# Performance work log

Measured on AMD Instinct MI355X. Metric: run time of the kernel, lower is better.

## Reference

```python
import jax, jax.numpy as jnp
import numpy as np

WIDTH = 64
N_LAYERS = 4
K_MAX = 16
DT = 0.05
EPS = 1e-5


def _gelu(x):
    return jax.nn.gelu(x, approximate=False)  # torch nn.GELU default = exact erf


def _pconv(x, w, b):
    # 1x1 conv: x (B,Cin,H,W), w (Cout,Cin), b (Cout,)
    return jnp.einsum('oc,bchw->bohw', w, x) + b[None, :, None, None]


def _spectral_conv(x, wr, wi):
    # Faithful to the original buggy einsum: x_ft is summed over ky before the weight multiply.
    B, C, H, W = x.shape
    x_ft = jnp.fft.rfft2(x, norm='ortho')              # (B,C,H,W//2+1) complex
    k = min(K_MAX, H, W // 2 + 1)
    weights = (wr + 1j * wi)[:, :, :k, :k]             # (Cin,Cout,k,k)
    S = jnp.sum(x_ft[:, :, :k, :k], axis=2)           # (B,Cin,k): sum over ky rows (broadcasted label j)
    blk = jnp.einsum('bik,ijkm->bjkm', S, weights.astype(x_ft.dtype))  # (B,Cout,k,k)
    out_ft = jnp.zeros((B, wr.shape[1], H, W // 2 + 1), dtype=x_ft.dtype)
    out_ft = out_ft.at[:, :, :k, :k].set(blk)
    return jnp.fft.irfft2(out_ft, s=(H, W), norm='ortho')


def _instance_norm(x):
    # InstanceNorm2d(affine=False): per (b,c) normalization over H,W, biased var
    mu = jnp.mean(x, axis=(2, 3), keepdims=True)
    var = jnp.var(x, axis=(2, 3), keepdims=True)
    return (x - mu) * jax.lax.rsqrt(var + EPS)


def _spectral_divergence(J):
    B, _, H, W = J.shape
    Jx_ft = jnp.fft.rfft2(J[:, 0:1], norm='ortho')
    Jy_ft = jnp.fft.rfft2(J[:, 1:2], norm='ortho')
    kx = jnp.fft.fftfreq(W, d=1.0 / W)[: W // 2 + 1]   # integer freqs, cols
    ky = jnp.fft.fftfreq(H, d=1.0 / H)[:H]             # integer freqs, rows
    # torch: kxx,kyy = meshgrid(ky,kx,'ij'); div_ft = 1j*kxx*Jx_ft + 1j*kyy*Jy_ft
    div_ft = 1j * ky[None, None, :, None] * Jx_ft + 1j * kx[None, None, None, :] * Jy_ft
    return jnp.fft.irfft2(div_ft, s=(H, W), norm='ortho')


def setup_inputs() -> dict:
    key = jax.random.key(0)
    ks = jax.random.split(key, 16)
    B, H, W = 8, 256, 256
    scale = 1.0 / (WIDTH * WIDTH)
    return {
        'state': jax.random.normal(ks[0], (B, 3, H, W), jnp.float32),
        'lift_w': 0.1 * jax.random.normal(ks[1], (WIDTH, 3), jnp.float32),
        'lift_b': jnp.zeros((WIDTH,), jnp.float32),
        'sw_real': scale * jax.random.normal(ks[2], (N_LAYERS, WIDTH, WIDTH, K_MAX, K_MAX), jnp.float32),
        'sw_imag': scale * jax.random.normal(ks[3], (N_LAYERS, WIDTH, WIDTH, K_MAX, K_MAX), jnp.float32),
        'pw_w': 0.05 * jax.random.normal(ks[4], (N_LAYERS, WIDTH, WIDTH), jnp.float32),
        'pw_b': jnp.zeros((N_LAYERS, WIDTH), jnp.float32),
        'flux_w1': 0.05 * jax.random.normal(ks[5], (WIDTH, WIDTH), jnp.float32),
        'flux_b1': jnp.zeros((WIDTH,), jnp.float32),
        'flux_w2': 0.05 * jax.random.normal(ks[6], (2, WIDTH), jnp.float32),
        'flux_b2': jnp.zeros((2,), jnp.float32),
        'pol_w1': 0.05 * jax.random.normal(ks[7], (WIDTH, WIDTH), jnp.float32),
        'pol_b1': jnp.zeros((WIDTH,), jnp.float32),
        'pol_w2': 0.05 * jax.random.normal(ks[8], (2, WIDTH), jnp.float32),
        'pol_b2': jnp.zeros((2,), jnp.float32),
    }


def reference(state, lift_w, lift_b, sw_real, sw_imag, pw_w, pw_b,
              flux_w1, flux_b1, flux_w2, flux_b2,
              pol_w1, pol_b1, pol_w2, pol_b2):
    x = _gelu(_pconv(state, lift_w, lift_b))
    for l in range(N_LAYERS):
        res = x
        x = _spectral_conv(x, sw_real[l], sw_imag[l])
        x = _pconv(x, pw_w[l], pw_b[l])
        x = _instance_norm(x)
        x = _gelu(x)
        x = x + res
    J = _pconv(_gelu(_pconv(x, flux_w1, flux_b1)), flux_w2, flux_b2)      # (B,2,H,W)
    dt_rho = -_spectral_divergence(J)                                     # (B,1,H,W)
    dt_P = _pconv(_gelu(_pconv(x, pol_w1, pol_b1)), pol_w2, pol_b2)       # (B,2,H,W)
    dt_state = jnp.concatenate([dt_rho, dt_P], axis=1)
    rho_new = state[:, 0:1] + DT * dt_rho
    P_new = state[:, 1:] + DT * dt_P
    rho_new = jnp.logaddexp(0.0, 10.0 * rho_new) / 10.0  # softplus(beta=10)
    state_pred = jnp.concatenate([rho_new, P_new], axis=1)
    return state_pred, dt_state
```

## Files before the change

### kernel.cpp

```cpp
#include <hip/hip_runtime.h>
#include <math.h>

#define HW 65536
#define TH_ 0.024543692606170259f

typedef __attribute__((ext_vector_type(8))) short bf16x8;
typedef __attribute__((ext_vector_type(4))) float f32x4;

__device__ __forceinline__ float gelu_f(float v){
    float u = fabsf(v)*0.7071067811865476f;
    float t = __builtin_amdgcn_rcpf(fmaf(0.3275911f, u, 1.0f));
    float p = t*fmaf(t, fmaf(t, fmaf(t, fmaf(t, 1.061405429f, -1.453152027f),
                     1.421413741f), -0.284496736f), 0.254829592f);
    float e = __expf(-u*u);
    float erfu = fmaf(-p, e, 1.0f);
    float er = copysignf(erfu, v);
    return 0.5f*v*(1.0f+er);
}

__device__ __forceinline__ short f2bf(float f){
    union { float f; unsigned u; } v; v.f = f;
    unsigned r = (v.u + 0x7FFF + ((v.u >> 16) & 1)) >> 16;
    return (short)r;
}
__device__ __forceinline__ float bf2f(short s){
    union { float f; unsigned u; } v; v.u = ((unsigned)(unsigned short)s) << 16;
    return v.f;
}

__device__ __forceinline__ unsigned cvt_pk_bf16(float lo, float hi){
    unsigned r;
    asm("v_cvt_pk_bf16_f32 %0, %1, %2" : "=v"(r) : "v"(lo), "v"(hi));
    return r;
}

union U8 { bf16x8 v; unsigned u[4]; };

__device__ __forceinline__ void split8(const float* f, bf16x8& H, bf16x8& L){
    U8 h, l;
    #pragma unroll
    for (int p=0;p<4;++p){
        float a = f[2*p], b = f[2*p+1];
        unsigned hp = cvt_pk_bf16(a, b);
        union { unsigned u; float fl; } ua, ub;
        ua.u = hp << 16; ub.u = hp & 0xffff0000u;
        h.u[p] = hp;
        l.u[p] = cvt_pk_bf16(a - ua.fl, b - ub.fl);
    }
    H = h.v; L = l.v;
}

__device__ __forceinline__ void s_partial_atomic(float TrT, float TiT, int w, int lane,
                                                 float* __restrict__ Sdst){
    float c1, s1; sincosf((float)w * TH_, &s1, &c1);
    float Sr[16], Si[16];
    float ck = 1.f, sk = 0.f;
    #pragma unroll
    for (int k=0;k<16;++k){
        Sr[k] = (TrT*ck + TiT*sk) * (1.0f/256.0f);
        Si[k] = (TiT*ck - TrT*sk) * (1.0f/256.0f);
        float nc = ck*c1 - sk*s1;
        sk = ck*s1 + sk*c1;
        ck = nc;
    }
    #pragma unroll
    for (int k=0;k<16;++k){
        #pragma unroll
        for (int off=32; off; off>>=1){
            Sr[k] += __shfl_xor(Sr[k], off, 64);
            Si[k] += __shfl_xor(Si[k], off, 64);
        }
    }
    if (lane < 32){
        float val = (lane & 1) ? Si[lane>>1] : Sr[lane>>1];
        atomicAdd(Sdst + lane, val);
    }
}

__global__ __launch_bounds__(256) void k_init(const float* __restrict__ fw1, const float* __restrict__ qw1,
                                              float* __restrict__ Wf, float* __restrict__ GH,
                                              float* __restrict__ KQ){
    if (blockIdx.x == 4){
        int h = threadIdx.x;
        double gr = 0.0, gi = 0.0;
        for (int ky=0; ky<16; ++ky){
            double a = -2.0*3.14159265358979323846*(double)(ky*h)/256.0;
            gr += cos(a); gi += sin(a);
        }
        GH[2*h] = (float)gr; GH[2*h+1] = (float)gi;
        double kk = 0.0, qq = 0.0;
        for (int k=1; k<128; ++k){
            double s = sin(2.0*3.14159265358979323846*(double)(k*h)/256.0);
            kk += (double)k * s;
            qq += s;
        }
        KQ[h]     = (float)(-kk/128.0);
        KQ[256+h] = (float)( qq/128.0);
        return;
    }
    int t = blockIdx.x*256 + threadIdx.x;
    int lane = t & 63, ks = (t>>6)&1, n = (t>>7)&3, ph = (t>>9)&1;
    int l15 = lane & 15, lg = lane >> 4;
    const float* w1p = ph ? qw1 : fw1;
    int oc = n*16 + l15;
    U8 h, l;
    #pragma unroll
    for (int p=0;p<4;++p){
        float a = w1p[oc*64 + ks*32 + lg*8 + 2*p];
        float b = w1p[oc*64 + ks*32 + lg*8 + 2*p+1];
        short ha = f2bf(a), hb = f2bf(b);
        h.u[p] = ((unsigned)(unsigned short)ha) | (((unsigned)(unsigned short)hb)<<16);
        short la = f2bf(a - bf2f(ha)), lb = f2bf(b - bf2f(hb));
        l.u[p] = ((unsigned)(unsigned short)la) | (((unsigned)(unsigned short)lb)<<16);
    }
    int idx = ((ph*4+n)*2+ks)*64 + lane;
    ((bf16x8*)Wf)[idx] = h.v;
    ((bf16x8*)Wf)[1024 + idx] = l.v;
}

__global__ __launch_bounds__(1024) void k_lift2(const float* __restrict__ st, const float* __restrict__ lw,
                                                const float* __restrict__ lb, const float* __restrict__ GH,
                                                float* __restrict__ x, float* __restrict__ Sout){
    int b = blockIdx.x >> 6, c = blockIdx.x & 63;
    int t = threadIdx.x;
    int w = t & 255, hq = t >> 8;
    __shared__ float sGH[512];
    __shared__ float2 tp[4][256];
    if (t < 512) sGH[t] = GH[t];
    __syncthreads();
    float l0 = lw[c*3], l1 = lw[c*3+1], l2 = lw[c*3+2], lbc = lb[c];
    const float* s0p = st + (size_t)(b*3)*HW;
    float* xp = x + (size_t)blockIdx.x*HW;
    float Tr = 0.f, Ti = 0.f;
    #pragma unroll 4
    for (int i=0; i<64; ++i){
        int h = hq*64 + i;
        int idx = h*256 + w;
        float v = fmaf(l0, s0p[idx], fmaf(l1, s0p[HW+idx], fmaf(l2, s0p[2*HW+idx], lbc)));
        v = gelu_f(v);
        xp[idx] = v;
        Tr = fmaf(sGH[2*h],   v, Tr);
        Ti = fmaf(sGH[2*h+1], v, Ti);
    }
    tp[hq][w] = make_float2(Tr, Ti);
    __syncthreads();
    if (hq == 0){
        float2 a = tp[0][w], b2 = tp[1][w], cc = tp[2][w], d = tp[3][w];
        float TrT = a.x+b2.x+cc.x+d.x, TiT = a.y+b2.y+cc.y+d.y;
        s_partial_atomic(TrT, TiT, w, t & 63, Sout + blockIdx.x*32);
    }
}

__global__ __launch_bounds__(256) void k_mixA(const float* __restrict__ S, const float* __restrict__ wr,
                                              const float* __restrict__ wi, float* __restrict__ A){
    int j = blockIdx.x >> 3, b = blockIdx.x & 7;
    __shared__ float sS[2048];
    for (int t=threadIdx.x; t<2048; t+=256) sS[t] = S[b*2048 + t];
    __syncthreads();
    int km = threadIdx.x, k = km >> 4;
    float ar = 0.f, ai = 0.f;
    const float* wrp = wr + j*256 + km;
    const float* wip = wi + j*256 + km;
    #pragma unroll 4
    for (int i=0;i<64;++i){
        float wrv = wrp[i*16384];
        float wiv = wip[i*16384];
        float2 sv = ((const float2*)sS)[i*16 + k];
        ar += sv.x*wrv - sv.y*wiv;
        ai += sv.x*wiv + sv.y*wrv;
    }
    ((float2*)A)[(b*64 + j)*256 + km] = make_float2(ar, ai);
}

__global__ __launch_bounds__(256) void k_mixB(const float* __restrict__ A, const float* __restrict__ pw,
                                              float* __restrict__ CS){
    int b = blockIdx.x >> 6, o = blockIdx.x & 63;
    int km = threadIdx.x, m = km & 15;
    const float2* Ap = (const float2*)A + b*64*256 + km;
    const float* pwp = pw + o*64;
    float cr=0.f, ci=0.f;
    #pragma unroll 4
    for (int j=0;j<64;++j){
        float p = pwp[j];
        float2 a = Ap[j*256];
        cr = fmaf(p, a.x, cr);
        ci = fmaf(p, a.y, ci);
    }
    float aw = (m==0)? 1.f : 4.f;
    float s = (km==0)? 0.f : aw*(cr*cr + ci*ci);
    #pragma unroll
    for (int off=32; off; off>>=1) s += __shfl_xor(s, off, 64);
    __shared__ float rsum[4];
    __shared__ float sinv;
    if ((threadIdx.x & 63) == 0) rsum[threadIdx.x>>6] = s;
    __syncthreads();
    if (threadIdx.x == 0){
        float var = (rsum[0]+rsum[1]+rsum[2]+rsum[3]) * (1.0f/131072.0f);
        sinv = rsqrtf(var + 1e-5f);
    }
    __syncthreads();
    float alpha = (m==0)? 1.f : 2.f;
    float sc = sinv * alpha * (1.0f/256.0f);
    if (km == 0) cr = 0.f;
    ((float2*)CS)[blockIdx.x*256 + km] = make_float2(cr*sc, ci*sc);
}

template<bool EMIT_S>
__global__ __launch_bounds__(256) void k_synth(const float* __restrict__ CS, float* __restrict__ x,
                                               const float* __restrict__ GH, float* __restrict__ Sout){
    int bo = blockIdx.x >> 2, wt = blockIdx.x & 3;
    int lane = threadIdx.x & 63, wv = threadIdx.x >> 6;
    int w = wt*64 + lane;
    __shared__ float sGH[512];
    __shared__ float2 sV[16][64];
    if (EMIT_S){
        sGH[threadIdx.x] = GH[threadIdx.x];
        sGH[256+threadIdx.x] = GH[256+threadIdx.x];
    }
    const float2* cs = (const float2*)CS + bo*256;
    {
        float Vr[4] = {0.f,0.f,0.f,0.f}, Vi[4] = {0.f,0.f,0.f,0.f};
        float stepc, steps; sincosf((float)w*TH_, &steps, &stepc);
        float pc = 1.f, ps = 0.f;
        for (int m=0;m<16;++m){
            #pragma unroll
            for (int kk=0;kk<4;++kk){
                float2 a = cs[(wv*4+kk)*16 + m];
                Vr[kk] += a.x*pc - a.y*ps;
                Vi[kk] += a.x*ps + a.y*pc;
            }
            float nc = pc*stepc - ps*steps;
            ps = pc*steps + ps*stepc;
            pc = nc;
        }
        #pragma unroll
        for (int kk=0;kk<4;++kk) sV[wv*4+kk][lane] = make_float2(Vr[kk], Vi[kk]);
    }
    __syncthreads();
    int h0 = wv*16;
    float rc[16], rs[16], qr[16], qi[16];
    #pragma unroll
    for (int k=0;k<16;++k){
        float2 v = sV[k][lane];
        sincosf((float)k*TH_, &rs[k], &rc[k]);
        float c0, s0; sincosf((float)(k*h0)*TH_, &s0, &c0);
        qr[k] = v.x*c0 - v.y*s0;
        qi[k] = v.x*s0 + v.y*c0;
    }
    float* xp = x + ((size_t)bo << 16);
    float Tr = 0.f, Ti = 0.f;
    for (int i=0;i<16;++i){
        float y0=0.f,y1=0.f,y2=0.f,y3=0.f;
        #pragma unroll
        for (int k=0;k<16;++k){
            float re = qr[k], im = qi[k];
            y0 += re;
            if ((k&3)==0)      { y1 += re; y2 += re; y3 += re; }
            else if ((k&3)==1) { y1 -= im; y2 -= re; y3 += im; }
            else if ((k&3)==2) { y1 -= re; y2 += re; y3 -= re; }
            else               { y1 += im; y2 -= re; y3 -= im; }
        }
        #pragma unroll
        for (int k=1;k<16;++k){
            float nr = qr[k]*rc[k] - qi[k]*rs[k];
            qi[k]    = qr[k]*rs[k] + qi[k]*rc[k];
            qr[k] = nr;
        }
        int p0 = (h0+i)*256 + w;
        float x0 = xp[p0], x1 = xp[p0+16384], x2 = xp[p0+32768], x3 = xp[p0+49152];
        float n0 = gelu_f(y0) + x0;
        float n1 = gelu_f(y1) + x1;
        float n2 = gelu_f(y2) + x2;
        float n3 = gelu_f(y3) + x3;
        xp[p0]       = n0;
        xp[p0+16384] = n1;
        xp[p0+32768] = n2;
        xp[p0+49152] = n3;
        if (EMIT_S){
            int h = h0+i;
            Tr = fmaf(sGH[2*h],     n0, Tr);  Ti = fmaf(sGH[2*h+1],     n0, Ti);
            Tr = fmaf(sGH[2*h+128], n1, Tr);  Ti = fmaf(sGH[2*h+129],   n1, Ti);
            Tr = fmaf(sGH[2*h+256], n2, Tr);  Ti = fmaf(sGH[2*h+257],   n2, Ti);
            Tr = fmaf(sGH[2*h+384], n3, Tr);  Ti = fmaf(sGH[2*h+385],   n3, Ti);
        }
    }
    if (EMIT_S){
        __shared__ float2 tpart[4][64];
        tpart[wv][lane] = make_float2(Tr, Ti);
        __syncthreads();
        if (wv == 0){
            float2 a = tpart[0][lane], b2 = tpart[1][lane];
            float2 c = tpart[2][lane], d = tpart[3][lane];
            float TrT = a.x+b2.x+c.x+d.x, TiT = a.y+b2.y+c.y+d.y;
            s_partial_atomic(TrT, TiT, w, lane, Sout + bo*32);
        }
    }
}

__global__ __launch_bounds__(256) void k_heads(const float* __restrict__ x,
        const float* __restrict__ Wf, const float* __restrict__ st,
        const float* __restrict__ fb1, const float* __restrict__ fw2, const float* __restrict__ fb2,
        const float* __restrict__ qb1, const float* __restrict__ qw2, const float* __restrict__ qb2,
        float* __restrict__ J, float* __restrict__ outp){
    __shared__ bf16x8 sWf[2048];
    for (int t = threadIdx.x; t < 2048; t += 256)
        sWf[t] = ((const bf16x8*)Wf)[t];
    __syncthreads();

    int wv = threadIdx.x >> 6, lane = threadIdx.x & 63;
    int l15 = lane & 15, lg = lane >> 4;
    int px0 = blockIdx.x*128 + wv*32;
    int b = px0 >> 16;
    int hwbase = px0 & (HW-1);
    const float* xb = x + (size_t)b*64*HW;

    bf16x8 Ahi[2][2], Alo[2][2];
    #pragma unroll
    for (int mt=0; mt<2; ++mt){
        int px = hwbase + mt*16 + l15;
        #pragma unroll
        for (int ks=0; ks<2; ++ks){
            float f[8];
            #pragma unroll
            for (int j=0; j<8; ++j)
                f[j] = xb[(size_t)((ks*32 + lg*8 + j))*HW + px];
            split8(f, Ahi[mt][ks], Alo[mt][ks]);
        }
    }

    #pragma unroll
    for (int ph=0; ph<2; ++ph){
        const float* b1p = ph ? qb1 : fb1;
        const float* w2p = ph ? qw2 : fw2;
        const float* b2p = ph ? qb2 : fb2;

        float p0[8], p1[8];
        #pragma unroll
        for (int t=0;t<8;++t){ p0[t]=0.f; p1[t]=0.f; }

        for (int n=0; n<4; ++n){
            int oc = n*16 + l15;
            float bias = b1p[oc];
            float w2a = w2p[oc], w2b = w2p[64+oc];
            int base = ((ph*4+n)*2)*64 + lane;
            bf16x8 Bhi0 = sWf[base];
            bf16x8 Bhi1 = sWf[base + 64];
            bf16x8 Blo0 = sWf[1024 + base];
            bf16x8 Blo1 = sWf[1024 + base + 64];
            #pragma unroll
            for (int mt=0; mt<2; ++mt){
                f32x4 d = {0.f,0.f,0.f,0.f};
                d = __builtin_amdgcn_mfma_f32_16x16x32_bf16(Ahi[mt][0], Bhi0, d, 0,0,0);
                d = __builtin_amdgcn_mfma_f32_16x16x32_bf16(Ahi[mt][0], Blo0, d, 0,0,0);
                d = __builtin_amdgcn_mfma_f32_16x16x32_bf16(Alo[mt][0], Bhi0, d, 0,0,0);
                d = __builtin_amdgcn_mfma_f32_16x16x32_bf16(Ahi[mt][1], Bhi1, d, 0,0,0);
                d = __builtin_amdgcn_mfma_f32_16x16x32_bf16(Ahi[mt][1], Blo1, d, 0,0,0);
                d = __builtin_amdgcn_mfma_f32_16x16x32_bf16(Alo[mt][1], Bhi1, d, 0,0,0);
                #pragma unroll
                for (int r=0;r<4;++r){
                    float g = gelu_f(d[r] + bias);
                    p0[mt*4+r] = fmaf(w2a, g, p0[mt*4+r]);
                    p1[mt*4+r] = fmaf(w2b, g, p1[mt*4+r]);
                }
            }
        }
        #pragma unroll
        for (int t=0;t<8;++t){
            #pragma unroll
            for (int off=1; off<16; off<<=1){
                p0[t] += __shfl_xor(p0[t], off, 64);
                p1[t] += __shfl_xor(p1[t], off, 64);
            }
        }
        float bo0 = b2p[0], bo1 = b2p[1];
        if (ph == 0){
            if (l15 == 0){
                float* plane = J + ((size_t)(b*2 + 0))*HW;
                #pragma unroll
                for (int mt=0; mt<2; ++mt){
                    int px = hwbase + mt*16 + lg*4;
                    float4 v; v.x=p0[mt*4+0]+bo0; v.y=p0[mt*4+1]+bo0; v.z=p0[mt*4+2]+bo0; v.w=p0[mt*4+3]+bo0;
                    *(float4*)(plane + px) = v;
                }
            } else if (l15 == 1){
                float* plane = J + ((size_t)(b*2 + 1))*HW;
                #pragma unroll
                for (int mt=0; mt<2; ++mt){
                    int px = hwbase + mt*16 + lg*4;
                    float4 v; v.x=p1[mt*4+0]+bo1; v.y=p1[mt*4+1]+bo1; v.z=p1[mt*4+2]+bo1; v.w=p1[mt*4+3]+bo1;
                    *(float4*)(plane + px) = v;
                }
            }
        } else {
            if (l15 < 2){
                const float* pv = (l15==0)? p0 : p1;
                float bN = (l15==0)? bo0 : bo1;
                const float* plane_st  = st   + ((size_t)(b*3+1+l15))*HW;
                float* plane_pred      = outp + ((size_t)(b*3+1+l15))*HW;
                float* plane_dt        = outp + 1572864 + ((size_t)(b*3+1+l15))*HW;
                #pragma unroll
                for (int mt=0; mt<2; ++mt){
                    int px = hwbase + mt*16 + lg*4;
                    float4 sv = *(const float4*)(plane_st + px);
                    float4 dt, pd;
                    dt.x = pv[mt*4+0]+bN; dt.y = pv[mt*4+1]+bN;
                    dt.z = pv[mt*4+2]+bN; dt.w = pv[mt*4+3]+bN;
                    pd.x = fmaf(0.05f, dt.x, sv.x); pd.y = fmaf(0.05f, dt.y, sv.y);
                    pd.z = fmaf(0.05f, dt.z, sv.z); pd.w = fmaf(0.05f, dt.w, sv.w);
                    *(float4*)(plane_pred + px) = pd;
                    *(float4*)(plane_dt + px)   = dt;
                }
            }
        }
    }
}

__global__ __launch_bounds__(256) void k_convH(const float* __restrict__ J, const float* __restrict__ KQ,
                                               float* __restrict__ Dx, float* __restrict__ r){
    int b = blockIdx.x >> 5, wt = blockIdx.x & 31;
    int w0 = wt*8;
    __shared__ float tile[256][12];
    __shared__ float sK[256];
    int t = threadIdx.x;
    sK[t] = KQ[t];
    {
        const float* rp = J + (size_t)(b*2)*HW + t*256 + w0;
        float4 a = *(const float4*)rp;
        float4 bb = *(const float4*)(rp+4);
        tile[t][0]=a.x;  tile[t][1]=a.y;  tile[t][2]=a.z;  tile[t][3]=a.w;
        tile[t][4]=bb.x; tile[t][5]=bb.y; tile[t][6]=bb.z; tile[t][7]=bb.w;
    }
    __syncthreads();
    if (t < 8){
        float acc = 0.f;
        for (int h=0; h<256; ++h) acc += (h & 1)? -tile[h][t] : tile[h][t];
        r[b*256 + w0 + t] = acc;
    }
    float o[8] = {0.f,0.f,0.f,0.f,0.f,0.f,0.f,0.f};
    for (int hp=0; hp<256; ++hp){
        float k = sK[(t - hp) & 255];
        float4 ra = *(const float4*)&tile[hp][0];
        float4 rb = *(const float4*)&tile[hp][4];
        o[0]=fmaf(k, ra.x, o[0]); o[1]=fmaf(k, ra.y, o[1]);
        o[2]=fmaf(k, ra.z, o[2]); o[3]=fmaf(k, ra.w, o[3]);
        o[4]=fmaf(k, rb.x, o[4]); o[5]=fmaf(k, rb.y, o[5]);
        o[6]=fmaf(k, rb.z, o[6]); o[7]=fmaf(k, rb.w, o[7]);
    }
    float* dp = Dx + (size_t)b*HW + t*256 + w0;
    float4 v0; v0.x=o[0]; v0.y=o[1]; v0.z=o[2]; v0.w=o[3];
    float4 v1; v1.x=o[4]; v1.y=o[5]; v1.z=o[6]; v1.w=o[7];
    *(float4*)dp = v0;
    *(float4*)(dp+4) = v1;
}

__global__ __launch_bounds__(256) void k_convW(const float* __restrict__ J, const float* __restrict__ KQ,
                                               const float* __restrict__ Dx, const float* __restrict__ r,
                                               const float* __restrict__ st, float* __restrict__ outp){
    int b = blockIdx.x >> 5, ht = blockIdx.x & 31;
    int h0 = ht*8;
    __shared__ float rows[8][256];
    __shared__ float sr[256], sK[256], sQ[256];
    int t = threadIdx.x;
    sK[t] = KQ[t];
    sQ[t] = KQ[256+t];
    sr[t] = r[b*256 + t];
    const float* jy = J + (size_t)(b*2+1)*HW;
    #pragma unroll
    for (int i=0;i<8;++i) rows[i][t] = jy[(h0+i)*256 + t];
    __syncthreads();
    float P = 0.f;
    float cv[8] = {0.f,0.f,0.f,0.f,0.f,0.f,0.f,0.f};
    for (int wp=0; wp<256; ++wp){
        int d = (t - wp) & 255;
        float kk = sK[d];
        P = fmaf(sQ[d], sr[wp], P);
        #pragma unroll
        for (int i=0;i<8;++i) cv[i] = fmaf(kk, rows[i][wp], cv[i]);
    }
    const float* s0p = st + (size_t)(b*3)*HW;
    const float* dxp = Dx + (size_t)b*HW;
    float* o_rho = outp + (size_t)(b*3)*HW;
    float* o_dt  = outp + 1572864 + (size_t)(b*3)*HW;
    #pragma unroll
    for (int i=0;i<8;++i){
        int h = h0 + i;
        int idx = h*256 + t;
        float corr = ((h & 1)? -0.5f : 0.5f) * P;
        float rho = -(dxp[idx] + cv[i] + corr);
        float tt = 10.f*fmaf(0.05f, rho, s0p[idx]);
        float sp = fmaxf(tt, 0.f) + log1pf(expf(-fabsf(tt)));
        o_rho[idx] = 0.1f*sp;
        o_dt[idx]  = rho;
    }
}

extern "C" void kernel_launch(void* const* d_in, const int* in_sizes, int n_in,
                              void* d_out, int out_size, void* d_ws, size_t ws_size,
                              hipStream_t stream){
    const float* state = (const float*)d_in[0];
    const float* lw  = (const float*)d_in[1];
    const float* lb  = (const float*)d_in[2];
    const float* swr = (const float*)d_in[3];
    const float* swi = (const float*)d_in[4];
    const float* pww = (const float*)d_in[5];
    const float* fw1 = (const float*)d_in[7];
    const float* fb1 = (const float*)d_in[8];
    const float* fw2 = (const float*)d_in[9];
    const float* fb2 = (const float*)d_in[10];
    const float* qw1 = (const float*)d_in[11];
    const float* qb1 = (const float*)d_in[12];
    const float* qw2 = (const float*)d_in[13];
    const float* qb2 = (const float*)d_in[14];
    float* outp = (float*)d_out;
    float* ws = (float*)d_ws;

    float* x   = ws;
    float* S   = x   + 33554432;
    float* A   = S   + 65536;
    float* CS  = A   + 262144;
    float* J   = CS  + 262144;
    float* Dx  = J   + 1048576;
    float* rr  = Dx  + 524288;
    float* GH  = rr  + 2048;
    float* KQ  = GH  + 512;
    float* Wf  = KQ  + 512;

    hipLaunchKernelGGL(k_init,  dim3(5), dim3(256), 0, stream, fw1, qw1, Wf, GH, KQ);
    hipMemsetAsync(S, 0, 65536*sizeof(float), stream);
    hipLaunchKernelGGL(k_lift2, dim3(512), dim3(1024), 0, stream, state, lw, lb, GH, x, S);
    for (int l=0; l<4; ++l){
        float* Sl = S + l*16384;
        hipLaunchKernelGGL(k_mixA, dim3(512), dim3(256), 0, stream, Sl,
                           swr + (size_t)l*1048576, swi + (size_t)l*1048576, A);
        hipLaunchKernelGGL(k_mixB, dim3(512), dim3(256), 0, stream, A, pww + l*4096, CS);
        if (l < 3)
            hipLaunchKernelGGL((k_synth<true>),  dim3(2048), dim3(256), 0, stream, CS, x, GH, S + (l+1)*16384);
        else
            hipLaunchKernelGGL((k_synth<false>), dim3(2048), dim3(256), 0, stream, CS, x, GH, S);
    }
    hipLaunchKernelGGL(k_heads, dim3(4096), dim3(256), 0, stream, x,
                       Wf, state, fb1, fw2, fb2, qb1, qw2, qb2, J, outp);
    hipLaunchKernelGGL(k_convH, dim3(256), dim3(256), 0, stream, J, KQ, Dx, rr);
    hipLaunchKernelGGL(k_convW, dim3(256), dim3(256), 0, stream, J, KQ, Dx, rr, state, outp);
}
```

Baseline: 479.8 us.

## Compute inverse row DFT in synth kernel with split-bf16 MFMA against precomputed twiddles

The per-thread rotating-phasor recurrence over 16 modes for the inverse H-direction transform in k_synth is replaced by 16x16x32 bf16 MFMAs. A precomputed cos/sin twiddle table, split into hi/lo bf16 parts, is multiplied against the mode coefficients using three MFMAs per tile to keep near-fp32 accuracy. The twiddle table is generated in extra k_init blocks and staged into LDS in every synth block. The change also remaps the thread-to-pixel layout and the S-partial reduction. It aims to cut VALU work in the synth stage, at the cost of extra LDS traffic and a different memory access pattern for x.

```diff
diff --git a/kernel.cpp b/kernel.cpp
--- a/kernel.cpp
+++ b/kernel.cpp
@@ -79,7 +79,7 @@
 
 __global__ __launch_bounds__(256) void k_init(const float* __restrict__ fw1, const float* __restrict__ qw1,
                                               float* __restrict__ Wf, float* __restrict__ GH,
-                                              float* __restrict__ KQ){
+                                              float* __restrict__ KQ, float* __restrict__ Tf){
     if (blockIdx.x == 4){
         int h = threadIdx.x;
         double gr = 0.0, gi = 0.0;
@@ -96,6 +96,32 @@
         }
         KQ[h]     = (float)(-kk/128.0);
         KQ[256+h] = (float)( qq/128.0);
+        return;
+    }
+    if (blockIdx.x >= 5){
+        int t2 = (blockIdx.x-5)*256 + threadIdx.x;
+        int mt = t2 >> 6, lane = t2 & 63;
+        int m = lane & 15, lg2 = lane >> 4;
+        int h = mt*16 + m;
+        U8 hi, lo;
+        #pragma unroll
+        for (int p=0;p<4;++p){
+            float vals[2];
+            #pragma unroll
+            for (int q=0;q<2;++q){
+                int kap = lg2*8 + 2*p + q;
+                int k = kap >> 1;
+                double a = 2.0*3.14159265358979323846*(double)(k*h)/256.0;
+                vals[q] = (kap & 1) ? (float)(-sin(a)) : (float)(cos(a));
+            }
+            short ha = f2bf(vals[0]), hb = f2bf(vals[1]);
+            hi.u[p] = ((unsigned)(unsigned short)ha) | (((unsigned)(unsigned short)hb)<<16);
+            short la = f2bf(vals[0] - bf2f(ha)), lb = f2bf(vals[1] - bf2f(hb));
+            lo.u[p] = ((unsigned)(unsigned short)la) | (((unsigned)(unsigned short)lb)<<16);
+        }
+        int idx = mt*64 + lane;
+        ((bf16x8*)Tf)[idx] = hi.v;
+        ((bf16x8*)Tf)[1024 + idx] = lo.v;
         return;
     }
     int t = blockIdx.x*256 + threadIdx.x;
@@ -207,20 +233,26 @@
 
 template<bool EMIT_S>
 __global__ __launch_bounds__(256) void k_synth(const float* __restrict__ CS, float* __restrict__ x,
-                                               const float* __restrict__ GH, float* __restrict__ Sout){
+                                               const float* __restrict__ GH, const float* __restrict__ Tf,
+                                               float* __restrict__ Sout){
     int bo = blockIdx.x >> 2, wt = blockIdx.x & 3;
     int lane = threadIdx.x & 63, wv = threadIdx.x >> 6;
-    int w = wt*64 + lane;
+    int l15 = lane & 15, lg = lane >> 4;
+    __shared__ bf16x8 sTf[2048];
     __shared__ float sGH[512];
-    __shared__ float2 sV[16][64];
+    __shared__ float2 sV[16][65];
+    __shared__ float2 stw[64];
+    for (int t = threadIdx.x; t < 2048; t += 256)
+        sTf[t] = ((const bf16x8*)Tf)[t];
     if (EMIT_S){
         sGH[threadIdx.x] = GH[threadIdx.x];
         sGH[256+threadIdx.x] = GH[256+threadIdx.x];
     }
     const float2* cs = (const float2*)CS + bo*256;
     {
+        int wA = wt*64 + lane;
         float Vr[4] = {0.f,0.f,0.f,0.f}, Vi[4] = {0.f,0.f,0.f,0.f};
-        float stepc, steps; sincosf((float)w*TH_, &steps, &stepc);
+        float stepc, steps; sincosf((float)wA*TH_, &steps, &stepc);
         float pc = 1.f, ps = 0.f;
         for (int m=0;m<16;++m){
             #pragma unroll
@@ -237,62 +269,48 @@
         for (int kk=0;kk<4;++kk) sV[wv*4+kk][lane] = make_float2(Vr[kk], Vi[kk]);
     }
     __syncthreads();
-    int h0 = wv*16;
-    float rc[16], rs[16], qr[16], qi[16];
-    #pragma unroll
-    for (int k=0;k<16;++k){
-        float2 v = sV[k][lane];
-        sincosf((float)k*TH_, &rs[k], &rc[k]);
-        float c0, s0; sincosf((float)(k*h0)*TH_, &s0, &c0);
-        qr[k] = v.x*c0 - v.y*s0;
-        qi[k] = v.x*s0 + v.y*c0;
+    int wloc = wv*16 + l15;
+    int w = wt*64 + wloc;
+    bf16x8 Bhi, Blo;
+    {
+        float f[8];
+        #pragma unroll
+        for (int j=0;j<8;++j){
+            int kap = lg*8 + j;
+            float2 v = sV[kap>>1][wloc];
+            f[j] = (kap & 1) ? v.y : v.x;
+        }
+        split8(f, Bhi, Blo);
     }
     float* xp = x + ((size_t)bo << 16);
     float Tr = 0.f, Ti = 0.f;
-    for (int i=0;i<16;++i){
-        float y0=0.f,y1=0.f,y2=0.f,y3=0.f;
-        #pragma unroll
-        for (int k=0;k<16;++k){
-            float re = qr[k], im = qi[k];
-            y0 += re;
-            if ((k&3)==0)      { y1 += re; y2 += re; y3 += re; }
-            else if ((k&3)==1) { y1 -= im; y2 -= re; y3 += im; }
-            else if ((k&3)==2) { y1 -= re; y2 += re; y3 -= re; }
-            else               { y1 += im; y2 -= re; y3 -= im; }
-        }
-        #pragma unroll
-        for (int k=1;k<16;++k){
-            float nr = qr[k]*rc[k] - qi[k]*rs[k];
-            qi[k]    = qr[k]*rs[k] + qi[k]*rc[k];
-            qr[k] = nr;
-        }
-        int p0 = (h0+i)*256 + w;
-        float x0 = xp[p0], x1 = xp[p0+16384], x2 = xp[p0+32768], x3 = xp[p0+49152];
-        float n0 = gelu_f(y0) + x0;
-        float n1 = gelu_f(y1) + x1;
-        float n2 = gelu_f(y2) + x2;
-        float n3 = gelu_f(y3) + x3;
-        xp[p0]       = n0;
-        xp[p0+16384] = n1;
-        xp[p0+32768] = n2;
-        xp[p0+49152] = n3;
-        if (EMIT_S){
-            int h = h0+i;
-            Tr = fmaf(sGH[2*h],     n0, Tr);  Ti = fmaf(sGH[2*h+1],     n0, Ti);
-            Tr = fmaf(sGH[2*h+128], n1, Tr);  Ti = fmaf(sGH[2*h+129],   n1, Ti);
-            Tr = fmaf(sGH[2*h+256], n2, Tr);  Ti = fmaf(sGH[2*h+257],   n2, Ti);
-            Tr = fmaf(sGH[2*h+384], n3, Tr);  Ti = fmaf(sGH[2*h+385],   n3, Ti);
+    for (int mt=0; mt<16; ++mt){
+        bf16x8 Ahi = sTf[mt*64 + lane];
+        bf16x8 Alo = sTf[1024 + mt*64 + lane];
+        f32x4 d = {0.f,0.f,0.f,0.f};
+        d = __builtin_amdgcn_mfma_f32_16x16x32_bf16(Ahi, Bhi, d, 0,0,0);
+        d = __builtin_amdgcn_mfma_f32_16x16x32_bf16(Ahi, Blo, d, 0,0,0);
+        d = __builtin_amdgcn_mfma_f32_16x16x32_bf16(Alo, Bhi, d, 0,0,0);
+        #pragma unroll
+        for (int r=0;r<4;++r){
+            int h = mt*16 + lg*4 + r;
+            int idx = h*256 + w;
+            float n = gelu_f(d[r]) + xp[idx];
+            xp[idx] = n;
+            if (EMIT_S){
+                Tr = fmaf(sGH[2*h],   n, Tr);
+                Ti = fmaf(sGH[2*h+1], n, Ti);
+            }
         }
     }
     if (EMIT_S){
-        __shared__ float2 tpart[4][64];
-        tpart[wv][lane] = make_float2(Tr, Ti);
+        Tr += __shfl_xor(Tr, 16, 64);  Tr += __shfl_xor(Tr, 32, 64);
+        Ti += __shfl_xor(Ti, 16, 64);  Ti += __shfl_xor(Ti, 32, 64);
+        if (lg == 0) stw[wloc] = make_float2(Tr, Ti);
         __syncthreads();
         if (wv == 0){
-            float2 a = tpart[0][lane], b2 = tpart[1][lane];
-            float2 c = tpart[2][lane], d = tpart[3][lane];
-            float TrT = a.x+b2.x+c.x+d.x, TiT = a.y+b2.y+c.y+d.y;
-            s_partial_atomic(TrT, TiT, w, lane, Sout + bo*32);
+            float2 tv = stw[lane];
+            s_partial_atomic(tv.x, tv.y, wt*64 + lane, lane, Sout + bo*32);
         }
     }
 }
@@ -524,8 +542,9 @@
     float* GH  = rr  + 2048;
     float* KQ  = GH  + 512;
     float* Wf  = KQ  + 512;
-
-    hipLaunchKernelGGL(k_init,  dim3(5), dim3(256), 0, stream, fw1, qw1, Wf, GH, KQ);
+    float* Tf  = Wf  + 8192;
+
+    hipLaunchKernelGGL(k_init,  dim3(9), dim3(256), 0, stream, fw1, qw1, Wf, GH, KQ, Tf);
     hipMemsetAsync(S, 0, 65536*sizeof(float), stream);
     hipLaunchKernelGGL(k_lift2, dim3(512), dim3(1024), 0, stream, state, lw, lb, GH, x, S);
     for (int l=0; l<4; ++l){
@@ -534,9 +553,9 @@
                            swr + (size_t)l*1048576, swi + (size_t)l*1048576, A);
         hipLaunchKernelGGL(k_mixB, dim3(512), dim3(256), 0, stream, A, pww + l*4096, CS);
         if (l < 3)
-            hipLaunchKernelGGL((k_synth<true>),  dim3(2048), dim3(256), 0, stream, CS, x, GH, S + (l+1)*16384);
+            hipLaunchKernelGGL((k_synth<true>),  dim3(2048), dim3(256), 0, stream, CS, x, GH, Tf, S + (l+1)*16384);
         else
-            hipLaunchKernelGGL((k_synth<false>), dim3(2048), dim3(256), 0, stream, CS, x, GH, S);
+            hipLaunchKernelGGL((k_synth<false>), dim3(2048), dim3(256), 0, stream, CS, x, GH, Tf, S);
     }
     hipLaunchKernelGGL(k_heads, dim3(4096), dim3(256), 0, stream, x,
                        Wf, state, fb1, fw2, fb2, qb1, qw2, qb2, J, outp);
```

Result: slower. 547.5 us (+14.1%).
